# Optimization experiments

Measured on AMD Instinct MI355X. Metric: run time of the kernel, lower is better.

The kernel has to match this reference:

```python
import jax, jax.numpy as jnp
import numpy as np
from jax import lax

K = 3          # kernel_size
OUT = 256      # out_channels
IN_CPG = 256   # in_channels // groups
GROUPS = 1
STRIDE = 1
PAD = 1
DN = ('NCHW', 'OIHW', 'NCHW')


def _bounds(i, n, o):
    return int(np.floor(i * n / o)), int(np.ceil((i + 1) * n / o))


def adaptive_pool2d(x, o, reduce_fn):
    # Faithful torch AdaptiveAvg/MaxPool2d: static bin boundaries.
    H, W = x.shape[2], x.shape[3]
    rows = []
    for i in range(o):
        r0, r1 = _bounds(i, H, o)
        cells = []
        for j in range(o):
            c0, c1 = _bounds(j, W, o)
            cells.append(reduce_fn(x[:, :, r0:r1, c0:c1], axis=(2, 3)))
        rows.append(jnp.stack(cells, axis=-1))
    return jnp.stack(rows, axis=-2)  # (B, C, o, o)


def _gconv(x, w, fg, pad='VALID'):
    return lax.conv_general_dilated(x, w, (1, 1), pad,
                                    dimension_numbers=DN,
                                    feature_group_count=fg)


def setup_inputs() -> dict:
    key = jax.random.key(0)
    ks = jax.random.split(key, 7)
    s = 0.05
    return {
        'x':     jax.random.normal(ks[0], (32, 256, 56, 56), jnp.float32),
        'w1':    jax.random.normal(ks[1], (IN_CPG, GROUPS, 3, 3), jnp.float32) * s,
        'b1':    jax.random.normal(ks[2], (IN_CPG,), jnp.float32) * s,
        'w2':    jax.random.normal(ks[3], (OUT * IN_CPG, 1, 1, 1), jnp.float32) * s,
        'b2':    jax.random.normal(ks[4], (OUT * IN_CPG,), jnp.float32) * s,
        'w_att': jax.random.normal(ks[5], (OUT * IN_CPG, GROUPS, 3, 3), jnp.float32) * s,
        'b_att': jax.random.normal(ks[6], (OUT * IN_CPG,), jnp.float32) * s,
    }


def reference(x, w1, b1, w2, b2, w_att, b_att):
    B, C, H, W = x.shape
    # attention branch: maxpool -> grouped 3x3 conv -> sigmoid
    maxi = adaptive_pool2d(x, K + 2, jnp.max)                    # (B, C, K+2, K+2)
    att = _gconv(maxi, w_att, IN_CPG) + b_att[None, :, None, None]  # (B, OUT*IN_CPG, K, K)
    att = jax.nn.sigmoid(att).reshape(B * OUT, IN_CPG, K, K)
    # weight branch: avgpool -> depthwise 3x3 -> relu -> grouped 1x1
    avg = adaptive_pool2d(x, K + 2, jnp.mean)                    # (B, C, K+2, K+2)
    wgt = jax.nn.relu(_gconv(avg, w1, IN_CPG) + b1[None, :, None, None])  # (B, IN_CPG, K, K)
    wgt = _gconv(wgt, w2, IN_CPG) + b2[None, :, None, None]      # (B, OUT*IN_CPG, K, K)
    wgt = wgt.reshape(B * OUT, IN_CPG, K, K)
    # per-sample dynamic conv as grouped conv with batch-as-groups
    xg = x.reshape(1, B * C, H, W)
    out = lax.conv_general_dilated(xg, wgt * att, (STRIDE, STRIDE),
                                   [(PAD, PAD), (PAD, PAD)],
                                   dimension_numbers=DN,
                                   feature_group_count=GROUPS * B)
    return out.reshape(B, OUT, out.shape[-2], out.shape[-1])
```

## Files before the change

### kernel.cpp

```cpp
#include <hip/hip_runtime.h>
#include <hip/hip_bf16.h>

#define BATCH 32
#define CIN   256
#define OCH   256
#define HW    56
#define PW    58
#define PAREA (PW*PW)
#define PLANE (HW*HW)

typedef float float4v __attribute__((ext_vector_type(4)));
typedef short short8  __attribute__((ext_vector_type(8)));

__device__ __forceinline__ unsigned short f2bf(float f) {
  union { float f; unsigned u; } v; v.f = f;
  unsigned r = v.u + 0x7fffu + ((v.u >> 16) & 1u);
  return (unsigned short)(r >> 16);
}

__global__ __launch_bounds__(256) void pool_kernel(const float* __restrict__ x,
                                                   float* __restrict__ avgp,
                                                   float* __restrict__ maxp) {
  __shared__ float plane[PLANE];
  int bc = blockIdx.x;
  const float* src = x + (size_t)bc * PLANE;
  for (int e = threadIdx.x; e < PLANE; e += 256) plane[e] = src[e];
  __syncthreads();
  if (threadIdx.x < 25) {
    int i = threadIdx.x / 5, j = threadIdx.x % 5;
    int r0 = (i * HW) / 5, r1 = ((i + 1) * HW + 4) / 5;
    int c0 = (j * HW) / 5, c1 = ((j + 1) * HW + 4) / 5;
    float s = 0.f, m = -1e30f;
    for (int r = r0; r < r1; ++r)
      for (int c = c0; c < c1; ++c) {
        float v = plane[r * HW + c];
        s += v; m = fmaxf(m, v);
      }
    avgp[(size_t)bc * 25 + threadIdx.x] = s / (float)((r1 - r0) * (c1 - c0));
    maxp[(size_t)bc * 25 + threadIdx.x] = m;
  }
}

__global__ __launch_bounds__(256) void wcalc_kernel(
    const float* __restrict__ avgp, const float* __restrict__ maxp,
    const float* __restrict__ w1, const float* __restrict__ b1,
    const float* __restrict__ w2, const float* __restrict__ b2,
    const float* __restrict__ watt, const float* __restrict__ batt,
    unsigned short* __restrict__ Wbf) {
  int blk = blockIdx.x;
  int oc = blk & 255, b = blk >> 8;
  __shared__ float s_avg[25], s_max[25], s_w1[9], s_wgt1[9];
  int tid = threadIdx.x;
  size_t base = ((size_t)b * 256 + oc) * 25;
  if (tid < 25) { s_avg[tid] = avgp[base + tid]; s_max[tid] = maxp[base + tid]; }
  if (tid >= 32 && tid < 41) s_w1[tid - 32] = w1[oc * 9 + (tid - 32)];
  __syncthreads();
  if (tid < 9) {
    int ky = tid / 3, kx = tid % 3;
    float acc = b1[oc];
    for (int u = 0; u < 3; ++u)
      for (int v = 0; v < 3; ++v)
        acc += s_avg[(ky + u) * 5 + kx + v] * s_w1[u * 3 + v];
    s_wgt1[tid] = fmaxf(acc, 0.f);
  }
  __syncthreads();
  int ic = tid;
  size_t g = (size_t)oc * 256 + ic;
  float wa[9];
#pragma unroll
  for (int r = 0; r < 9; ++r) wa[r] = watt[g * 9 + r];
  float ba = batt[g], w2v = w2[g], b2v = b2[g];
#pragma unroll
  for (int r = 0; r < 9; ++r) {
    int ky = r / 3, kx = r % 3;
    float s = ba;
#pragma unroll
    for (int u = 0; u < 3; ++u)
#pragma unroll
      for (int v = 0; v < 3; ++v)
        s += s_max[(ky + u) * 5 + kx + v] * wa[u * 3 + v];
    float att = 1.f / (1.f + __expf(-s));
    float wv = (s_wgt1[r] * w2v + b2v) * att;
    Wbf[(((size_t)b * 9 + r) * 256 + oc) * 256 + ic] = f2bf(wv);
  }
}

__global__ __launch_bounds__(256) void border_kernel(unsigned short* __restrict__ xp) {
  int bid = blockIdx.x;
  int b = bid / 228, bi = bid % 228;
  int pos;
  if (bi < 58)       pos = bi;
  else if (bi < 116) pos = 57 * PW + (bi - 58);
  else if (bi < 172) pos = (bi - 116 + 1) * PW;
  else               pos = (bi - 172 + 1) * PW + 57;
  xp[((size_t)b * PAREA + pos) * 256 + threadIdx.x] = 0;
}

__global__ __launch_bounds__(256) void xprep_kernel(const float* __restrict__ x,
                                                    unsigned short* __restrict__ xp) {
  int bid = blockIdx.x;
  int y = bid % 56; int t2 = bid / 56; int icb = t2 & 3; int b = t2 >> 2;
  __shared__ float tr[56][65];
  for (int e = threadIdx.x; e < 56 * 64; e += 256) {
    int icl = e / 56, col = e % 56;
    tr[col][icl] = x[((size_t)(b * 256 + icb * 64 + icl)) * PLANE + y * HW + col];
  }
  __syncthreads();
  for (int e = threadIdx.x; e < 448; e += 256) {
    int col = e >> 3, c8 = e & 7;
    short8 v;
#pragma unroll
    for (int k = 0; k < 8; ++k) v[k] = (short)f2bf(tr[col][c8 * 8 + k]);
    size_t dst = ((size_t)b * PAREA + (size_t)(y + 1) * PW + (col + 1)) * 256 + icb * 64 + c8 * 8;
    *(short8*)&xp[dst] = v;
  }
}

__global__ __launch_bounds__(256, 2) void conv_kernel(
    const unsigned short* __restrict__ xp,
    const unsigned short* __restrict__ Wbf,
    float* __restrict__ out) {
  __shared__ unsigned short bpl[348 * 32];
  __shared__ unsigned short apl[128 * 32];

  int bid = blockIdx.x;
  int rt = bid % 14; int t2 = bid / 14; int ocb = t2 & 1; int b = t2 >> 1;
  int y0 = rt * 4;
  int tid = threadIdx.x;
  int lane = tid & 63, w = tid >> 6;
  int mw = w & 1, nw = w >> 1;
  int quad = lane >> 4, l16 = lane & 15;

  int basepos[7];
#pragma unroll
  for (int nt = 0; nt < 7; ++nt) {
    int n = nw * 112 + nt * 16 + l16;
    basepos[nt] = (n / 56) * PW + (n % 56);
  }

  float4v acc[4][7];
#pragma unroll
  for (int mt = 0; mt < 4; ++mt)
#pragma unroll
    for (int nt = 0; nt < 7; ++nt)
      acc[mt][nt] = (float4v){0.f, 0.f, 0.f, 0.f};

  const size_t xbase = ((size_t)b * PAREA + (size_t)y0 * PW) * 256;

  for (int icb = 0; icb < 8; ++icb) {
    __syncthreads();
    for (int e = tid; e < 1392; e += 256) {
      int c = e & 3, p = e >> 2;
      *(short8*)&bpl[p * 32 + c * 8] =
          *(const short8*)&xp[xbase + (size_t)p * 256 + icb * 32 + c * 8];
    }
    for (int r = 0; r < 9; ++r) {
      __syncthreads();
      const size_t wbase = (((size_t)b * 9 + r) * 256 + ocb * 128) * 256 + icb * 32;
      for (int e = tid; e < 512; e += 256) {
        int c = e & 3, oc = e >> 2;
        *(short8*)&apl[oc * 32 + c * 8] =
            *(const short8*)&Wbf[wbase + (size_t)oc * 256 + c * 8];
      }
      __syncthreads();
      int ky = r / 3, kx = r - ky * 3;
      int poff = (ky * PW + kx) * 32;
      short8 bfrag[7];
#pragma unroll
      for (int nt = 0; nt < 7; ++nt)
        bfrag[nt] = *(const short8*)&bpl[basepos[nt] * 32 + poff + quad * 8];
#pragma unroll
      for (int mt = 0; mt < 4; ++mt) {
        short8 afrag = *(const short8*)&apl[(mw * 64 + mt * 16 + l16) * 32 + quad * 8];
#pragma unroll
        for (int nt = 0; nt < 7; ++nt)
          acc[mt][nt] = __builtin_amdgcn_mfma_f32_16x16x32_bf16(afrag, bfrag[nt], acc[mt][nt], 0, 0, 0);
      }
    }
  }

#pragma unroll
  for (int mt = 0; mt < 4; ++mt) {
    int m = ocb * 128 + mw * 64 + mt * 16 + quad * 4;
#pragma unroll
    for (int nt = 0; nt < 7; ++nt) {
      int n = nw * 112 + nt * 16 + l16;
      int yy = y0 + n / 56, xx = n % 56;
      size_t o = (((size_t)b * 256 + m) * 56 + yy) * 56 + xx;
#pragma unroll
      for (int reg = 0; reg < 4; ++reg)
        out[o + (size_t)reg * PLANE] = acc[mt][nt][reg];
    }
  }
}

extern "C" void kernel_launch(void* const* d_in, const int* in_sizes, int n_in,
                              void* d_out, int out_size, void* d_ws, size_t ws_size,
                              hipStream_t stream) {
  const float* x    = (const float*)d_in[0];
  const float* w1   = (const float*)d_in[1];
  const float* b1   = (const float*)d_in[2];
  const float* w2   = (const float*)d_in[3];
  const float* b2   = (const float*)d_in[4];
  const float* watt = (const float*)d_in[5];
  const float* batt = (const float*)d_in[6];
  float* out = (float*)d_out;

  float* avgp = (float*)d_ws;
  float* maxp = avgp + 204800;
  unsigned short* Wbf = (unsigned short*)(maxp + 204800);
  unsigned short* xp  = Wbf + (size_t)32 * 9 * 256 * 256;

  pool_kernel<<<BATCH * CIN, 256, 0, stream>>>(x, avgp, maxp);
  wcalc_kernel<<<BATCH * OCH, 256, 0, stream>>>(avgp, maxp, w1, b1, w2, b2, watt, batt, Wbf);
  border_kernel<<<BATCH * 228, 256, 0, stream>>>(xp);
  xprep_kernel<<<BATCH * 4 * 56, 256, 0, stream>>>(x, xp);
  conv_kernel<<<BATCH * 2 * 14, 256, 0, stream>>>(xp, Wbf, out);
}
```

Measured before the change: 453.8 us.

## Double-buffer conv LDS tiles via global_load_lds with swizzled layouts

The conv kernel now double-buffers its A (weight) and B (input) LDS tiles and fills them with direct global-to-LDS loads issued one step ahead, so memory traffic overlaps the MFMA work. This cuts the syncs per step from two to one. The weight and padded-input producers write pre-tiled, XOR-swizzled layouts so fragment reads avoid LDS bank conflicts and each weight tile is one contiguous block. Block indices are remapped to change scheduling order across CUs. The price is twice the LDS per block, which may lower occupancy, plus a tighter coupling between producer layouts and the consumer.

```diff
diff --git a/kernel.cpp b/kernel.cpp
--- a/kernel.cpp
+++ b/kernel.cpp
@@ -16,6 +16,13 @@
   union { float f; unsigned u; } v; v.f = f;
   unsigned r = v.u + 0x7fffu + ((v.u >> 16) & 1u);
   return (unsigned short)(r >> 16);
+}
+
+__device__ __forceinline__ void gll16(const unsigned short* g, unsigned short* l) {
+  __builtin_amdgcn_global_load_lds(
+      (const __attribute__((address_space(1))) void*)g,
+      (__attribute__((address_space(3))) void*)l,
+      16, 0, 0);
 }
 
 __global__ __launch_bounds__(256) void pool_kernel(const float* __restrict__ x,
@@ -70,6 +77,14 @@
 #pragma unroll
   for (int r = 0; r < 9; ++r) wa[r] = watt[g * 9 + r];
   float ba = batt[g], w2v = w2[g], b2v = b2[g];
+
+  int ocb = oc >> 7, ocl = oc & 127;
+  int sa = (ocl >> 1) & 3;
+  int icb = ic >> 5, c = (ic >> 3) & 3, sub = ic & 7;
+  int cph = c ^ sa;
+  size_t tilebase = ((size_t)((b * 2 + ocb) * 8 + icb)) * 9;
+  size_t elem = (size_t)ocl * 32 + cph * 8 + sub;
+
 #pragma unroll
   for (int r = 0; r < 9; ++r) {
     int ky = r / 3, kx = r % 3;
@@ -81,7 +96,7 @@
         s += s_max[(ky + u) * 5 + kx + v] * wa[u * 3 + v];
     float att = 1.f / (1.f + __expf(-s));
     float wv = (s_wgt1[r] * w2v + b2v) * att;
-    Wbf[(((size_t)b * 9 + r) * 256 + oc) * 256 + ic] = f2bf(wv);
+    Wbf[(tilebase + r) * 4096 + elem] = f2bf(wv);
   }
 }
 
@@ -111,7 +126,10 @@
     short8 v;
 #pragma unroll
     for (int k = 0; k < 8; ++k) v[k] = (short)f2bf(tr[col][c8 * 8 + k]);
-    size_t dst = ((size_t)b * PAREA + (size_t)(y + 1) * PW + (col + 1)) * 256 + icb * 64 + c8 * 8;
+    int pos = (y + 1) * PW + (col + 1);
+    int sb = (pos >> 1) & 3;
+    int c8p = (c8 & 4) | ((c8 & 3) ^ sb);
+    size_t dst = ((size_t)b * PAREA + pos) * 256 + icb * 64 + c8p * 8;
     *(short8*)&xp[dst] = v;
   }
 }
@@ -120,11 +138,12 @@
     const unsigned short* __restrict__ xp,
     const unsigned short* __restrict__ Wbf,
     float* __restrict__ out) {
-  __shared__ unsigned short bpl[348 * 32];
-  __shared__ unsigned short apl[128 * 32];
-
-  int bid = blockIdx.x;
-  int rt = bid % 14; int t2 = bid / 14; int ocb = t2 & 1; int b = t2 >> 1;
+  __shared__ unsigned short bpl[2][348 * 32];
+  __shared__ unsigned short apl[2][128 * 32];
+
+  int p = blockIdx.x;
+  int L = (p & 7) * 112 + (p >> 3);
+  int rt = L % 14; int t2 = L / 14; int ocb = t2 & 1; int b = t2 >> 1;
   int y0 = rt * 4;
   int tid = threadIdx.x;
   int lane = tid & 63, w = tid >> 6;
@@ -137,6 +156,7 @@
     int n = nw * 112 + nt * 16 + l16;
     basepos[nt] = (n / 56) * PW + (n % 56);
   }
+  const int sa_off = (quad ^ ((l16 >> 1) & 3)) << 3;
 
   float4v acc[4][7];
 #pragma unroll
@@ -146,36 +166,44 @@
       acc[mt][nt] = (float4v){0.f, 0.f, 0.f, 0.f};
 
   const size_t xbase = ((size_t)b * PAREA + (size_t)y0 * PW) * 256;
-
+  const unsigned short* wb = Wbf + (size_t)((b * 2 + ocb) * 72) * 4096;
+
+  for (int e = tid; e < 1392; e += 256)
+    gll16(&xp[xbase + (size_t)(e >> 2) * 256 + (e & 3) * 8], &bpl[0][e * 8]);
+  for (int e = tid; e < 512; e += 256)
+    gll16(&wb[e * 8], &apl[0][e * 8]);
+  __syncthreads();
+
+  int kk = 0;
   for (int icb = 0; icb < 8; ++icb) {
-    __syncthreads();
-    for (int e = tid; e < 1392; e += 256) {
-      int c = e & 3, p = e >> 2;
-      *(short8*)&bpl[p * 32 + c * 8] =
-          *(const short8*)&xp[xbase + (size_t)p * 256 + icb * 32 + c * 8];
-    }
-    for (int r = 0; r < 9; ++r) {
-      __syncthreads();
-      const size_t wbase = (((size_t)b * 9 + r) * 256 + ocb * 128) * 256 + icb * 32;
-      for (int e = tid; e < 512; e += 256) {
-        int c = e & 3, oc = e >> 2;
-        *(short8*)&apl[oc * 32 + c * 8] =
-            *(const short8*)&Wbf[wbase + (size_t)oc * 256 + c * 8];
-      }
-      __syncthreads();
+    for (int r = 0; r < 9; ++r, ++kk) {
+      if (kk < 71) {
+        const unsigned short* asrc = wb + (size_t)(kk + 1) * 4096;
+        for (int e = tid; e < 512; e += 256)
+          gll16(&asrc[e * 8], &apl[(kk + 1) & 1][e * 8]);
+      }
+      if (icb < 7 && r < 6) {
+        int e = r * 256 + tid;
+        if (e < 1392)
+          gll16(&xp[xbase + (size_t)(e >> 2) * 256 + (icb + 1) * 32 + (e & 3) * 8],
+                &bpl[(icb + 1) & 1][e * 8]);
+      }
       int ky = r / 3, kx = r - ky * 3;
-      int poff = (ky * PW + kx) * 32;
+      int po = ky * PW + kx;
       short8 bfrag[7];
 #pragma unroll
-      for (int nt = 0; nt < 7; ++nt)
-        bfrag[nt] = *(const short8*)&bpl[basepos[nt] * 32 + poff + quad * 8];
+      for (int nt = 0; nt < 7; ++nt) {
+        int pr = basepos[nt] + po;
+        bfrag[nt] = *(const short8*)&bpl[icb & 1][pr * 32 + ((quad ^ ((pr >> 1) & 3)) << 3)];
+      }
 #pragma unroll
       for (int mt = 0; mt < 4; ++mt) {
-        short8 afrag = *(const short8*)&apl[(mw * 64 + mt * 16 + l16) * 32 + quad * 8];
+        short8 afrag = *(const short8*)&apl[kk & 1][(mw * 64 + mt * 16 + l16) * 32 + sa_off];
 #pragma unroll
         for (int nt = 0; nt < 7; ++nt)
           acc[mt][nt] = __builtin_amdgcn_mfma_f32_16x16x32_bf16(afrag, bfrag[nt], acc[mt][nt], 0, 0, 0);
       }
+      __syncthreads();
     }
   }
 
```

After: 661.9 us. 1.46x slower.
